# Kernel tuning notes

Measured on AMD Instinct MI355X. Metric: run time of the kernel, lower is better.

Reference implementation:

```python
import jax, jax.numpy as jnp
import numpy as np

H = 4            # attention heads
D_SUB = 32       # per-head hidden dim
D_HID = H * D_SUB
B = 100          # graphs in batch
N_PER = 5000     # nodes per graph
N = B * N_PER
DEG = 16         # avg degree
E = N * DEG
K_PER = 2500     # ceil(0.5 * N_PER), pooling_rate=0.5


def setup_inputs() -> dict:
    key = jax.random.key(0)
    k0, k1, k2, k3 = jax.random.split(key, 4)
    x = jax.random.normal(k0, (N, D_HID), jnp.float32)
    sub_xs = jax.random.normal(k1, (H, N, D_SUB), jnp.float32)
    # edges strictly within each graph (contiguous node blocks per graph)
    rng = np.random.default_rng(0)
    src = rng.integers(0, N_PER, size=(B, N_PER * DEG))
    dst = rng.integers(0, N_PER, size=(B, N_PER * DEG))
    off = (np.arange(B) * N_PER)[:, None]
    edge_index = jnp.asarray(
        np.stack([(src + off).reshape(-1), (dst + off).reshape(-1)]), jnp.int32)
    batch = jnp.repeat(jnp.arange(B, dtype=jnp.int32), N_PER)
    att_W = jax.random.normal(k2, (H, D_SUB, 1), jnp.float32) * 0.1
    att_b = jnp.zeros((H, 1), jnp.float32)
    score_W = jax.random.normal(k3, (1, 1), jnp.float32)
    score_b = jnp.zeros((1,), jnp.float32)
    return {"x": x, "sub_xs": sub_xs, "att_W": att_W, "att_b": att_b,
            "score_W": score_W, "score_b": score_b,
            "edge_index": edge_index, "batch": batch}


def _gcn_prop(h, row, col, dis):
    # PyG GCNConv propagation with self-loops: D^{-1/2}(A+I)D^{-1/2} h
    norm = (dis[row] * dis[col])[:, None]                       # [E,1]
    agg = jax.ops.segment_sum(h[row] * norm, col, num_segments=N)
    return agg + h * (dis ** 2)[:, None]                        # self-loop term deg^-1


def reference(x, sub_xs, att_W, att_b, score_W, score_b, edge_index, batch):
    row, col = edge_index[0], edge_index[1]
    deg = 1.0 + jax.ops.segment_sum(jnp.ones((E,), x.dtype), col, num_segments=N)
    dis = deg ** -0.5
    # per-head GCNConv(sub_hidden, 1): [H,N,1]
    h = jnp.einsum('hnd,hdo->hno', sub_xs, att_W)
    agg = jax.vmap(lambda hh: _gcn_prop(hh, row, col, dis))(h) + att_b[:, None, :]
    # torch F.softmax with implicit dim=1 on [N,1] -> softmax over size-1 axis (all ones); faithful
    att = jax.nn.softmax(agg, axis=-1)                          # [H,N,1]
    pool = att.mean(axis=0)                                     # 'mean' att pooling -> [N,1]
    # pooling_score_layer = GCNConv(1,1)
    score = (_gcn_prop(pool @ score_W, row, col, dis) + score_b)[:, 0]  # [N]
    # batched topk: equal-size contiguous graphs -> static k per graph
    _, idx = jax.lax.top_k(score.reshape(B, N_PER), K_PER)      # sorted desc per graph
    perm = (idx + (jnp.arange(B) * N_PER)[:, None]).reshape(-1) # [B*K_PER]
    x_new = x[perm] * jnp.tanh(score[perm])[:, None]            # global att weighting
    batch_new = batch[perm]
    # filter_adj: keep edges with both endpoints selected, reindex to new ids
    n_idx = jnp.full((N,), -1, jnp.int32).at[perm].set(
        jnp.arange(B * K_PER, dtype=jnp.int32))
    r, c = n_idx[row], n_idx[col]
    keep = (r >= 0) & (c >= 0)
    pos = jnp.nonzero(keep, size=E, fill_value=0)[0]            # compacted, order-preserving
    valid = jnp.arange(E) < keep.sum()
    edge_new = jnp.stack([jnp.where(valid, r[pos], -1),
                          jnp.where(valid, c[pos], -1)])        # [2,E], -1 padded
    return x_new, edge_new, batch_new, perm
```

## Files before the change

kernel.cpp:

```cpp
#include <hip/hip_runtime.h>
#include <hip/hip_bf16.h>

constexpr int H      = 4;
constexpr int D_SUB  = 32;
constexpr int D_HID  = 128;
constexpr int B      = 100;
constexpr int N_PER  = 5000;
constexpr int N      = B * N_PER;
constexpr int DEG    = 16;
constexpr int E      = N * DEG;
constexpr int E_PER  = N_PER * DEG;
constexpr int K_PER  = 2500;
constexpr int NK     = B * K_PER;

constexpr int EPB    = 4096;
constexpr int EPT    = 16;
constexpr int NBLK_E = (E + EPB - 1) / EPB;

constexpr int SUBR   = 625;
constexpr int LCAP   = 11640;

constexpr int M      = 8192;

constexpr unsigned long long FLG_A = 1ull << 62;
constexpr unsigned long long FLG_I = 2ull << 62;

__device__ __forceinline__ int swz8(int bid, int chunk) {
    return (bid & 7) * chunk + (bid >> 3);
}

__device__ __forceinline__ int ph(int i) { return i + (i >> 3); }

__global__ __launch_bounds__(1024) void k_count(const int* __restrict__ col,
                                                int* __restrict__ cnt2) {
    __shared__ int h[N_PER];
    int lb = swz8(blockIdx.x, 25);
    int g = lb >> 1, half = lb & 1;
    for (int i = threadIdx.x; i < N_PER; i += 1024) h[i] = 0;
    __syncthreads();
    int ebase = g * E_PER + half * (E_PER / 2);
    int nbase = g * N_PER;
    const int4* c4 = (const int4*)(col + ebase);
    for (int i = threadIdx.x; i < E_PER / 2 / 4; i += 1024) {
        int4 v = c4[i];
        atomicAdd(&h[v.x - nbase], 1);
        atomicAdd(&h[v.y - nbase], 1);
        atomicAdd(&h[v.z - nbase], 1);
        atomicAdd(&h[v.w - nbase], 1);
    }
    __syncthreads();
    int* dst = cnt2 + half * N + nbase;
    for (int i = threadIdx.x; i < N_PER; i += 1024) dst[i] = h[i];
}

__global__ void k_dis(const int* __restrict__ cnt2, int* __restrict__ cnt,
                      float* __restrict__ dis) {
    int v = blockIdx.x * blockDim.x + threadIdx.x;
    if (v < N) {
        int c = cnt2[v] + cnt2[N + v];
        cnt[v] = c;
        float d = (float)(1 + c);
        dis[v] = __fdiv_rn(1.0f, __fsqrt_rn(d));
    }
}

__global__ __launch_bounds__(1024) void k_score_fused(const int* __restrict__ row,
                                                      const int* __restrict__ col,
                                                      const int* __restrict__ cnt,
                                                      const float* __restrict__ dis,
                                                      const float* __restrict__ scW,
                                                      const float* __restrict__ scB,
                                                      float* __restrict__ score) {
    __shared__ float dis_l[N_PER];
    __shared__ int   wsum[16];
    __shared__ int   offs_l[SUBR];
    __shared__ int   curs_l[SUBR];
    __shared__ int   list[LCAP];
    int lb = swz8(blockIdx.x, 100);
    int g = lb >> 3, q = lb & 7;
    int t = threadIdx.x;
    int nbase = g * N_PER;
    int ebase = g * E_PER;
    int lo = q * SUBR;

    const float4* d4 = (const float4*)(dis + nbase);
    for (int j4 = t; j4 < N_PER / 4; j4 += 1024) {
        float4 dv4 = d4[j4];
        int j = 4 * j4;
        dis_l[j]     = dv4.x;
        dis_l[j + 1] = dv4.y;
        dis_l[j + 2] = dv4.z;
        dis_l[j + 3] = dv4.w;
    }

    int v = (t < SUBR) ? cnt[nbase + lo + t] : 0;
    int lane = t & 63, wid = t >> 6;
    int x = v;
#pragma unroll
    for (int s = 1; s < 64; s <<= 1) {
        int o = __shfl_up(x, s, 64);
        if (lane >= s) x += o;
    }
    if (lane == 63) wsum[wid] = x;
    __syncthreads();
    if (wid == 0) {
        int ws = (lane < 16) ? wsum[lane] : 0;
#pragma unroll
        for (int s = 1; s < 16; s <<= 1) {
            int o = __shfl_up(ws, s, 64);
            if (lane >= s) ws += o;
        }
        if (lane < 16) wsum[lane] = ws;
    }
    __syncthreads();
    int incl = x + (wid > 0 ? wsum[wid - 1] : 0);
    if (t < SUBR) { offs_l[t] = incl - v + t; curs_l[t] = 0; }
    __syncthreads();

    const int4* c4 = (const int4*)(col + ebase);
    const int4* r4 = (const int4*)(row + ebase);
    for (int i4 = t; i4 < E_PER / 4; i4 += 1024) {
        int4 cv = c4[i4];
        int4 rv = r4[i4];
        int i0 = 4 * i4;
#pragma unroll
        for (int m = 0; m < 4; m++) {
            int cl = ((m == 0) ? cv.x : (m == 1) ? cv.y : (m == 2) ? cv.z : cv.w) - nbase;
            int rl = ((m == 0) ? rv.x : (m == 1) ? rv.y : (m == 2) ? rv.z : rv.w) - nbase;
            unsigned d = (unsigned)(cl - lo);
            if (d < (unsigned)SUBR) {
                int i = i0 + m;
                int slot = atomicAdd(&curs_l[d], 1);
                int pos = offs_l[d] + slot;
                if (pos < LCAP) list[pos] = (i << 13) | rl;
            }
        }
    }
    __syncthreads();

    if (t < SUBR) {
        int base = offs_l[t];
        int k = v;
        if (base + k > LCAP) k = 0;
        for (int i = 1; i < k; i++) {
            int key = list[base + i];
            int j = i - 1;
            while (j >= 0 && list[base + j] > key) { list[base + j + 1] = list[base + j]; j--; }
            list[base + j + 1] = key;
        }
        float w = scW[0];
        float dv = dis_l[lo + t];
        float s = 0.0f;
        for (int i = 0; i < k; i++) {
            int rl = list[base + i] & 8191;
            s = __fadd_rn(s, __fmul_rn(w, __fmul_rn(dis_l[rl], dv)));
        }
        s = __fadd_rn(s, __fmul_rn(w, __fmul_rn(dv, dv)));
        s = __fadd_rn(s, scB[0]);
        score[nbase + lo + t] = s;
    }
}

__global__ __launch_bounds__(1024) void k_topk(const float* __restrict__ score,
                                               float* __restrict__ out_batch,
                                               float* __restrict__ out_perm,
                                               int* __restrict__ perm_i,
                                               int* __restrict__ n_idx) {
    __shared__ unsigned long long keys[M + (M >> 3)];
    int b = blockIdx.x, t = threadIdx.x;
    int base = 8 * t;

    unsigned long long v[8];
    if (t < 625) {
        const float4* s4 = (const float4*)(score + b * N_PER + base);
        float4 f0 = s4[0], f1 = s4[1];
        float fs[8] = {f0.x, f0.y, f0.z, f0.w, f1.x, f1.y, f1.z, f1.w};
#pragma unroll
        for (int m = 0; m < 8; m++) {
            unsigned u = __float_as_uint(fs[m]);
            unsigned asc = u ^ ((u & 0x80000000u) ? 0xFFFFFFFFu : 0x80000000u);
            v[m] = ((unsigned long long)(~asc) << 32) | (unsigned)(base + m);
        }
    } else {
#pragma unroll
        for (int m = 0; m < 8; m++) v[m] = ~0ull;
    }

#define CEV(x, y, up) { if ((v[x] > v[y]) == (up)) { unsigned long long tmp = v[x]; v[x] = v[y]; v[y] = tmp; } }
    CEV(0, 1, true)  CEV(2, 3, false) CEV(4, 5, true)  CEV(6, 7, false)
    CEV(0, 2, true)  CEV(1, 3, true)  CEV(4, 6, false) CEV(5, 7, false)
    CEV(0, 1, true)  CEV(2, 3, true)  CEV(4, 5, false) CEV(6, 7, false)
    {
        bool u8 = ((t & 1) == 0);
        CEV(0, 4, u8) CEV(1, 5, u8) CEV(2, 6, u8) CEV(3, 7, u8)
        CEV(0, 2, u8) CEV(1, 3, u8) CEV(4, 6, u8) CEV(5, 7, u8)
        CEV(0, 1, u8) CEV(2, 3, u8) CEV(4, 5, u8) CEV(6, 7, u8)
    }
#pragma unroll
    for (int m = 0; m < 8; m++) keys[ph(base + m)] = v[m];
    __syncthreads();

    for (int k = 16; k <= M; k <<= 1) {
        bool last = (k == M);
        for (int j = k >> 1; j >= 8; j >>= 1) {
            int np = (last && j < (M >> 1)) ? (M >> 2) : (M >> 1);
            for (int p = t; p < np; p += 1024) {
                int i = ((p & ~(j - 1)) << 1) | (p & (j - 1));
                int ip = i | j;
                bool up = ((i & k) == 0);
                unsigned long long a = keys[ph(i)];
                unsigned long long c = keys[ph(ip)];
                if ((a > c) == up) { keys[ph(i)] = c; keys[ph(ip)] = a; }
            }
            __syncthreads();
        }
        int nb = last ? 512 : 1024;
        if (t < nb) {
            bool up = ((base & k) == 0);
            unsigned long long w[8];
#pragma unroll
            for (int m = 0; m < 8; m++) w[m] = keys[ph(base + m)];
#define CEW(x, y) { if ((w[x] > w[y]) == up) { unsigned long long tmp = w[x]; w[x] = w[y]; w[y] = tmp; } }
            CEW(0, 4) CEW(1, 5) CEW(2, 6) CEW(3, 7)
            CEW(0, 2) CEW(1, 3) CEW(4, 6) CEW(5, 7)
            CEW(0, 1) CEW(2, 3) CEW(4, 5) CEW(6, 7)
#pragma unroll
            for (int m = 0; m < 8; m++) keys[ph(base + m)] = w[m];
        }
        __syncthreads();
    }

    for (int r = t; r < K_PER; r += 1024) {
        unsigned long long key = keys[ph(r)];
        int idx = (int)(key & 0xFFFFFFFFull);
        int gl = b * N_PER + idx;
        int ni = b * K_PER + r;
        perm_i[ni] = gl;
        n_idx[gl] = ni;
        out_perm[ni] = (float)gl;
        out_batch[ni] = (float)b;
    }
}

__global__ void k_xnew(const float4* __restrict__ x4, const float* __restrict__ score,
                       const int* __restrict__ perm_i, float4* __restrict__ out4) {
    int tid = blockIdx.x * blockDim.x + threadIdx.x;
    if (tid >= NK * (D_HID / 4)) return;
    int i = tid >> 5;
    int c = tid & 31;
    int g = perm_i[i];
    float ts = tanhf(score[g]);
    float4 v = x4[(long)g * 32 + c];
    v.x *= ts; v.y *= ts; v.z *= ts; v.w *= ts;
    out4[tid] = v;
}

__global__ void k_prefill(float4* __restrict__ oe0, float4* __restrict__ oe1,
                          int4* __restrict__ n_idx4,
                          unsigned long long* __restrict__ status) {
    int i = blockIdx.x * blockDim.x + threadIdx.x;
    int stride = gridDim.x * blockDim.x;
    float4 m1 = make_float4(-1.0f, -1.0f, -1.0f, -1.0f);
    for (int j = i; j < E / 4; j += stride) { oe0[j] = m1; oe1[j] = m1; }
    int4 mi = make_int4(-1, -1, -1, -1);
    for (int j = i; j < N / 4; j += stride) n_idx4[j] = mi;
    for (int j = i; j < NBLK_E; j += stride) status[j] = 0ull;
}

__global__ __launch_bounds__(256) void k_compact(const int* __restrict__ row,
                                                 const int* __restrict__ col,
                                                 const int* __restrict__ n_idx,
                                                 unsigned long long* __restrict__ status,
                                                 float* __restrict__ oe0,
                                                 float* __restrict__ oe1) {
    __shared__ int sh[256];
    __shared__ int excl_sh;
    int blk = blockIdx.x, t = threadIdx.x;
    int base = blk * EPB + t * EPT;
    int rr[EPT], cc[EPT];
    int cnt = 0;
    if (blk < NBLK_E - 1) {
#pragma unroll
        for (int i4 = 0; i4 < 4; i4++) {
            int4 rv = ((const int4*)(row + base))[i4];
            int4 cv = ((const int4*)(col + base))[i4];
            rr[4 * i4 + 0] = n_idx[rv.x];  cc[4 * i4 + 0] = n_idx[cv.x];
            rr[4 * i4 + 1] = n_idx[rv.y];  cc[4 * i4 + 1] = n_idx[cv.y];
            rr[4 * i4 + 2] = n_idx[rv.z];  cc[4 * i4 + 2] = n_idx[cv.z];
            rr[4 * i4 + 3] = n_idx[rv.w];  cc[4 * i4 + 3] = n_idx[cv.w];
        }
#pragma unroll
        for (int i = 0; i < EPT; i++)
            if (rr[i] >= 0 && cc[i] >= 0) cnt++;
    } else {
#pragma unroll
        for (int i = 0; i < EPT; i++) {
            int e = base + i;
            int rv = -1, cv = -1;
            if (e < E) { rv = n_idx[row[e]]; cv = n_idx[col[e]]; }
            rr[i] = rv; cc[i] = cv;
            if (rv >= 0 && cv >= 0) cnt++;
        }
    }
    sh[t] = cnt;
    __syncthreads();
    for (int s = 1; s < 256; s <<= 1) {
        int a = (t >= s) ? sh[t - s] : 0;
        __syncthreads();
        sh[t] += a;
        __syncthreads();
    }
    int incl = sh[t];
    int agg  = sh[255];
    if (t == 0) {
        if (blk == 0) {
            atomicExch(&status[0], FLG_I | (unsigned long long)(unsigned)agg);
            excl_sh = 0;
        } else {
            atomicExch(&status[blk], FLG_A | (unsigned long long)(unsigned)agg);
            unsigned long long ex = 0;
            for (int i = blk - 1; i >= 0; i--) {
                unsigned long long sv;
                do { sv = atomicAdd(&status[i], 0ull); } while (sv == 0ull);
                ex += (sv & 0xFFFFFFFFull);
                if (sv & FLG_I) break;
            }
            atomicExch(&status[blk], FLG_I | (ex + (unsigned long long)(unsigned)agg));
            excl_sh = (int)ex;
        }
    }
    __syncthreads();
    int pos = excl_sh + incl - cnt;
#pragma unroll
    for (int i = 0; i < EPT; i++) {
        if (rr[i] >= 0 && cc[i] >= 0) {
            oe0[pos] = (float)rr[i];
            oe1[pos] = (float)cc[i];
            pos++;
        }
    }
}

extern "C" void kernel_launch(void* const* d_in, const int* in_sizes, int n_in,
                              void* d_out, int out_size, void* d_ws, size_t ws_size,
                              hipStream_t stream) {
    const float* x   = (const float*)d_in[0];
    const float* scW = (const float*)d_in[4];
    const float* scB = (const float*)d_in[5];
    const int*   edge = (const int*)d_in[6];
    const int*   row = edge;
    const int*   col = edge + E;

    unsigned long long* status = (unsigned long long*)d_ws;
    int*   ws_i    = (int*)(status + NBLK_E);
    int*   cnt2    = ws_i;
    int*   deg_cnt = ws_i + 2 * N;
    float* dis     = (float*)(ws_i + 3 * N);
    float* score   = (float*)(ws_i + 4 * N);
    int*   n_idx   = ws_i + 5 * N;
    int*   perm_i  = ws_i + 6 * N;

    float* out_x     = (float*)d_out;
    float* oe0       = out_x + (size_t)NK * D_HID;
    float* oe1       = oe0 + E;
    float* out_batch = oe1 + E;
    float* out_perm  = out_batch + NK;

    k_prefill<<<2048, 256, 0, stream>>>((float4*)oe0, (float4*)oe1, (int4*)n_idx, status);
    k_count<<<200, 1024, 0, stream>>>(col, cnt2);
    k_dis<<<(N + 255) / 256, 256, 0, stream>>>(cnt2, deg_cnt, dis);
    k_score_fused<<<800, 1024, 0, stream>>>(row, col, deg_cnt, dis, scW, scB, score);
    k_topk<<<B, 1024, 0, stream>>>(score, out_batch, out_perm, perm_i, n_idx);
    k_xnew<<<(NK * (D_HID / 4) + 255) / 256, 256, 0, stream>>>((const float4*)x, score, perm_i,
                                                               (float4*)out_x);
    k_compact<<<NBLK_E, 256, 0, stream>>>(row, col, n_idx, status, oe0, oe1);
}
```

Baseline: 258.0 us.

## Vectorize k_dis, epoch-barrier edge scan, and wave-shuffle scan in compact

k_dis now processes four nodes per thread using int4/float4 loads and stores. The edge bucketing loop in k_score_fused is split into 8 epochs with a block barrier after each, likely to keep waves in lockstep and improve cache locality of the streamed row/col reads. The block prefix sum in k_compact replaces an 8-step shared-memory Hillis-Steele scan with wavefront shuffles plus a small cross-wave combine. The epoch barriers add synchronization and may reorder atomic slot assignment, though the later sort keeps the result deterministic.

```diff
diff --git a/kernel.cpp b/kernel.cpp
--- a/kernel.cpp
+++ b/kernel.cpp
@@ -19,6 +19,8 @@
 
 constexpr int SUBR   = 625;
 constexpr int LCAP   = 11640;
+constexpr int NEPOCH = 8;
+constexpr int EP_I4  = (E_PER / 4) / NEPOCH;
 
 constexpr int M      = 8192;
 
@@ -53,14 +55,19 @@
     for (int i = threadIdx.x; i < N_PER; i += 1024) dst[i] = h[i];
 }
 
-__global__ void k_dis(const int* __restrict__ cnt2, int* __restrict__ cnt,
-                      float* __restrict__ dis) {
-    int v = blockIdx.x * blockDim.x + threadIdx.x;
-    if (v < N) {
-        int c = cnt2[v] + cnt2[N + v];
-        cnt[v] = c;
-        float d = (float)(1 + c);
-        dis[v] = __fdiv_rn(1.0f, __fsqrt_rn(d));
+__global__ void k_dis(const int4* __restrict__ cnt2a, const int4* __restrict__ cnt2b,
+                      int4* __restrict__ cnt, float4* __restrict__ dis) {
+    int i = blockIdx.x * blockDim.x + threadIdx.x;
+    if (i < N / 4) {
+        int4 a = cnt2a[i], b = cnt2b[i];
+        int4 c = make_int4(a.x + b.x, a.y + b.y, a.z + b.z, a.w + b.w);
+        cnt[i] = c;
+        float4 d;
+        d.x = __fdiv_rn(1.0f, __fsqrt_rn((float)(1 + c.x)));
+        d.y = __fdiv_rn(1.0f, __fsqrt_rn((float)(1 + c.y)));
+        d.z = __fdiv_rn(1.0f, __fsqrt_rn((float)(1 + c.z)));
+        d.w = __fdiv_rn(1.0f, __fsqrt_rn((float)(1 + c.w)));
+        dis[i] = d;
     }
 }
 
@@ -119,24 +126,26 @@
 
     const int4* c4 = (const int4*)(col + ebase);
     const int4* r4 = (const int4*)(row + ebase);
-    for (int i4 = t; i4 < E_PER / 4; i4 += 1024) {
-        int4 cv = c4[i4];
-        int4 rv = r4[i4];
-        int i0 = 4 * i4;
-#pragma unroll
-        for (int m = 0; m < 4; m++) {
-            int cl = ((m == 0) ? cv.x : (m == 1) ? cv.y : (m == 2) ? cv.z : cv.w) - nbase;
-            int rl = ((m == 0) ? rv.x : (m == 1) ? rv.y : (m == 2) ? rv.z : rv.w) - nbase;
-            unsigned d = (unsigned)(cl - lo);
-            if (d < (unsigned)SUBR) {
-                int i = i0 + m;
-                int slot = atomicAdd(&curs_l[d], 1);
-                int pos = offs_l[d] + slot;
-                if (pos < LCAP) list[pos] = (i << 13) | rl;
+    for (int ep = 0; ep < NEPOCH; ep++) {
+        for (int i4 = ep * EP_I4 + t; i4 < (ep + 1) * EP_I4; i4 += 1024) {
+            int4 cv = c4[i4];
+            int4 rv = r4[i4];
+            int i0 = 4 * i4;
+#pragma unroll
+            for (int m = 0; m < 4; m++) {
+                int cl = ((m == 0) ? cv.x : (m == 1) ? cv.y : (m == 2) ? cv.z : cv.w) - nbase;
+                int rl = ((m == 0) ? rv.x : (m == 1) ? rv.y : (m == 2) ? rv.z : rv.w) - nbase;
+                unsigned d = (unsigned)(cl - lo);
+                if (d < (unsigned)SUBR) {
+                    int i = i0 + m;
+                    int slot = atomicAdd(&curs_l[d], 1);
+                    int pos = offs_l[d] + slot;
+                    if (pos < LCAP) list[pos] = (i << 13) | rl;
+                }
             }
         }
-    }
-    __syncthreads();
+        __syncthreads();
+    }
 
     if (t < SUBR) {
         int base = offs_l[t];
@@ -273,7 +282,7 @@
                                                  unsigned long long* __restrict__ status,
                                                  float* __restrict__ oe0,
                                                  float* __restrict__ oe1) {
-    __shared__ int sh[256];
+    __shared__ int wsum[4];
     __shared__ int excl_sh;
     int blk = blockIdx.x, t = threadIdx.x;
     int base = blk * EPB + t * EPT;
@@ -302,16 +311,29 @@
             if (rv >= 0 && cv >= 0) cnt++;
         }
     }
-    sh[t] = cnt;
-    __syncthreads();
-    for (int s = 1; s < 256; s <<= 1) {
-        int a = (t >= s) ? sh[t - s] : 0;
+    int lane = t & 63, wid = t >> 6;
+    int x = cnt;
+#pragma unroll
+    for (int s = 1; s < 64; s <<= 1) {
+        int o = __shfl_up(x, s, 64);
+        if (lane >= s) x += o;
+    }
+    if (lane == 63) wsum[wid] = x;
+    __syncthreads();
+    if (t == 0) {
+        int a0 = wsum[0], a1 = wsum[1], a2 = wsum[2];
+        wsum[1] = a0; wsum[2] = a0 + a1; wsum[3] = a0 + a1 + a2;
+        wsum[0] = 0;
+    }
+    __syncthreads();
+    int incl = x + wsum[wid];
+    int agg;
+    {
+        __shared__ int agg_sh;
+        if (t == 255) agg_sh = incl;
         __syncthreads();
-        sh[t] += a;
-        __syncthreads();
-    }
-    int incl = sh[t];
-    int agg  = sh[255];
+        agg = agg_sh;
+    }
     if (t == 0) {
         if (blk == 0) {
             atomicExch(&status[0], FLG_I | (unsigned long long)(unsigned)agg);
@@ -368,7 +390,8 @@
 
     k_prefill<<<2048, 256, 0, stream>>>((float4*)oe0, (float4*)oe1, (int4*)n_idx, status);
     k_count<<<200, 1024, 0, stream>>>(col, cnt2);
-    k_dis<<<(N + 255) / 256, 256, 0, stream>>>(cnt2, deg_cnt, dis);
+    k_dis<<<(N / 4 + 255) / 256, 256, 0, stream>>>((const int4*)cnt2, (const int4*)(cnt2 + N),
+                                                   (int4*)deg_cnt, (float4*)dis);
     k_score_fused<<<800, 1024, 0, stream>>>(row, col, deg_cnt, dis, scW, scB, score);
     k_topk<<<B, 1024, 0, stream>>>(score, out_batch, out_perm, perm_i, n_idx);
     k_xnew<<<(NK * (D_HID / 4) + 255) / 256, 256, 0, stream>>>((const float4*)x, score, perm_i,
```

Result: no change. 256.1 us, median of 2 (-0.8%).
